# Kernel tuning notes

Measured on AMD Instinct MI355X. Metric: run time of the kernel, lower is better.

## Reference

```python
import jax, jax.numpy as jnp
import numpy as np

B, N, D_MODEL, H = 2, 512, 256, 8
DH, DS, DE = 8, 8, 8          # hyperbolic / spherical / euclidean component dims
HEAD = D_MODEL // H           # 32
HALF = HEAD // 2              # 16 rope frequencies
KAPPA_S = 1.0                 # spherical curvature
EPS = 1e-6


def setup_inputs() -> dict:
    key = jax.random.key(0)
    ks = jax.random.split(key, 10)
    h = jax.random.normal(ks[0], (B, N, D_MODEL), jnp.float32)
    # manifold coords: hyperbolic part inside Poincare ball, spherical part on unit sphere
    xh = 0.3 * jnp.tanh(jax.random.normal(ks[1], (B, N, DH), jnp.float32))
    xs_raw = jax.random.normal(ks[2], (B, N, DS), jnp.float32)
    xs = xs_raw / jnp.linalg.norm(xs_raw, axis=-1, keepdims=True)
    xe = jax.random.normal(ks[3], (B, N, DE), jnp.float32)
    x = jnp.concatenate([xh, xs, xe], axis=-1)
    def lin(k):
        return 0.05 * jax.random.normal(k, (D_MODEL, D_MODEL), jnp.float32)
    inp = dict(
        h=h, x=x,
        Wq=lin(ks[4]), bq=jnp.zeros((D_MODEL,), jnp.float32),
        Wk=lin(ks[5]), bk=jnp.zeros((D_MODEL,), jnp.float32),
        Wv=lin(ks[6]), bv=jnp.zeros((D_MODEL,), jnp.float32),
        Wo=lin(ks[7]), bo=jnp.zeros((D_MODEL,), jnp.float32),
        w_kernel=jnp.ones((H, 3), jnp.float32),   # torch init: ones(num_heads, num_comp)
        beta=jnp.ones((H,), jnp.float32),
        edge_bias=0.1 * jax.random.normal(ks[8], (B, 1, N, N), jnp.float32),
        node_mask=jnp.ones((B, N), bool),
    )
    return inp


def _pairwise_geometry(x):
    """Returns dh (B,N,N), sdot (B,N,N), de2 (B,N,N), dist (B,N,N)."""
    xh, xs, xe = x[..., :DH], x[..., DH:DH + DS], x[..., DH + DS:]
    # hyperbolic: Poincare-ball distance arccosh(1 + 2|a-b|^2 / ((1-|a|^2)(1-|b|^2)))
    dh2_num = jnp.sum((xh[:, :, None, :] - xh[:, None, :, :]) ** 2, -1)
    one_m = 1.0 - jnp.sum(xh * xh, -1)                               # (B,N)
    arg = 1.0 + 2.0 * dh2_num / (one_m[:, :, None] * one_m[:, None, :])
    dh = jnp.arccosh(jnp.maximum(arg, 1.0 + EPS))
    # spherical: arccos of dot (unit vectors); raw dot kept for the kernel term
    sdot = jnp.einsum('bnd,bmd->bnm', xs, xs)
    ds = jnp.arccos(jnp.clip(sdot, -1.0 + EPS, 1.0 - EPS)) / np.sqrt(KAPPA_S)
    # euclidean: squared distance (kernel uses -d^2; product dist uses d^2)
    de2 = jnp.sum((xe[:, :, None, :] - xe[:, None, :, :]) ** 2, -1)
    dist = jnp.sqrt(dh * dh + ds * ds + de2)
    return dh, sdot, de2, dist


def reference(h, x, Wq, bq, Wk, bk, Wv, bv, Wo, bo, w_kernel, beta, edge_bias, node_mask):
    scale = 1.0 / np.sqrt(HEAD)
    rope_freq = jnp.exp(-np.log(10000.0) * jnp.arange(HALF, dtype=jnp.float32) / HALF)

    def heads(t):  # (B,N,D) -> (B,H,N,head)
        return t.reshape(B, N, H, HEAD).transpose(0, 2, 1, 3)

    Q = heads(h @ Wq.T + bq)
    K = heads(h @ Wk.T + bk)
    V = heads(h @ Wv.T + bv)

    dh, sdot, de2, dist = _pairwise_geometry(x)

    # M-RoPE: rotate Q by pairwise angle theta_ij = omega * d_M(x_i, x_j)
    theta = dist[..., None] * rope_freq                  # (B,N,N,half)
    cos_t = jnp.cos(theta)[:, None]                      # (B,1,N,N,half)
    sin_t = jnp.sin(theta)[:, None]
    q1, q2 = Q[..., 0::2], Q[..., 1::2]                  # (B,H,N,half)
    k1, k2 = K[..., 0::2], K[..., 1::2]
    qk_same = q1[:, :, :, None, :] * k1[:, :, None, :, :] + q2[:, :, :, None, :] * k2[:, :, None, :, :]
    qk_cross = q1[:, :, :, None, :] * k2[:, :, None, :, :] - q2[:, :, :, None, :] * k1[:, :, None, :, :]
    attn = (cos_t * qk_same + sin_t * qk_cross).sum(-1) * scale   # (B,H,N,N)

    # geodesic kernel bias: per-component kernels [H:-d_H, S:k*a.b, E:-|a-b|^2]
    kernel_stack = jnp.stack([-dh, KAPPA_S * sdot, -de2], axis=-1)  # (B,N,N,3)
    geo = jnp.einsum('hc,bnmc->bhnm', w_kernel, kernel_stack)
    attn = attn + beta[None, :, None, None] * geo + edge_bias

    attn = jnp.where(node_mask[:, None, None, :], attn, -jnp.inf)
    p = jax.nn.softmax(attn, axis=-1)
    out = jnp.einsum('bhnm,bhmd->bhnd', p, V).transpose(0, 2, 1, 3).reshape(B, N, D_MODEL)
    return out @ Wo.T + bo
```

## Files before the change

### kernel.cpp

```cpp
#include <hip/hip_runtime.h>

#define N_TOK 512
#define NH 8

typedef __attribute__((ext_vector_type(8))) short short8;
typedef __attribute__((ext_vector_type(4))) short short4v;
typedef __attribute__((ext_vector_type(4))) float f32x4;

__device__ __forceinline__ unsigned short f2bf(float f) {
    union { float f; unsigned u; } v; v.f = f;
    return (unsigned short)((v.u + 0x7FFF + ((v.u >> 16) & 1)) >> 16);
}

__global__ __launch_bounds__(256) void gemm_qkv_mfma(
    const float* __restrict__ A,
    const float* __restrict__ Wq, const float* __restrict__ Wk, const float* __restrict__ Wv,
    const float* __restrict__ bq, const float* __restrict__ bk, const float* __restrict__ bv,
    float* __restrict__ Qb, float* __restrict__ KR, float* __restrict__ Vb)
{
    const int bx = blockIdx.x;
    const int t = threadIdx.x;
    const int z = bx >> 8, rem = bx & 255;
    const int m0 = (rem >> 3) * 32, n0 = (rem & 7) * 32;
    const float* W    = (z == 0) ? Wq : (z == 1) ? Wk : Wv;
    const float* bias = (z == 0) ? bq : (z == 1) ? bk : bv;

    __shared__ short As[32][264];
    __shared__ short Ws[32][264];

    #pragma unroll
    for (int r = 0; r < 8; ++r) {
        int idx = t + 256 * r;
        int row = idx >> 6, c4 = (idx & 63) * 4;
        float4 a = *(const float4*)&A[(m0 + row) * 256 + c4];
        short4v pa = {(short)f2bf(a.x), (short)f2bf(a.y), (short)f2bf(a.z), (short)f2bf(a.w)};
        *(short4v*)&As[row][c4] = pa;
        float4 w = *(const float4*)&W[(n0 + row) * 256 + c4];
        short4v pw = {(short)f2bf(w.x), (short)f2bf(w.y), (short)f2bf(w.z), (short)f2bf(w.w)};
        *(short4v*)&Ws[row][c4] = pw;
    }
    __syncthreads();

    const int w = t >> 6, lane = t & 63;
    const int wm = (w >> 1) * 16, wn = (w & 1) * 16;
    const int frow = lane & 15, kq = lane >> 4;

    f32x4 acc = {0.f, 0.f, 0.f, 0.f};
    #pragma unroll
    for (int k0 = 0; k0 < 8; ++k0) {
        short8 af = *(const short8*)&As[wm + frow][k0 * 32 + kq * 8];
        short8 wf = *(const short8*)&Ws[wn + frow][k0 * 32 + kq * 8];
        if (z == 1) acc = __builtin_amdgcn_mfma_f32_16x16x32_bf16(wf, af, acc, 0, 0, 0);
        else        acc = __builtin_amdgcn_mfma_f32_16x16x32_bf16(af, wf, acc, 0, 0, 0);
    }
    const int col = lane & 15, rq = (lane >> 4) * 4;
    if (z == 1) {
        int tok = m0 + wm + col;
        int bb = tok >> 9, j = tok & 511;
        #pragma unroll
        for (int r = 0; r < 4; ++r) {
            int d = n0 + wn + rq + r;
            int h = d >> 5, dd = d & 31, f = dd >> 1, r2 = dd & 1;
            KR[((size_t)bb * 128 + h * 16 + f) * 1024 + j * 2 + r2] = acc[r] + bias[d];
        }
    } else {
        float* C = (z == 0) ? Qb : Vb;
        float bsv = bias[n0 + wn + col];
        #pragma unroll
        for (int r = 0; r < 4; ++r)
            C[(m0 + wm + rq + r) * 256 + n0 + wn + col] = acc[r] + bsv;
    }
}

__global__ __launch_bounds__(256) void geo_kernel(
    const float* __restrict__ x, float* __restrict__ geo)
{
    const int j0 = blockIdx.x * 256;
    const int i  = blockIdx.y;
    const int b  = blockIdx.z;
    const int t  = threadIdx.x;

    __shared__ float xls[256 * 25];
    const float4* xsrc = (const float4*)(x + ((size_t)b * N_TOK + j0) * 24);
    #pragma unroll
    for (int r = 0; r < 6; ++r) {
        int idx = t + 256 * r;
        float4 v = xsrc[idx];
        int row = idx / 6, c = (idx % 6) * 4;
        float* dst = &xls[row * 25 + c];
        dst[0] = v.x; dst[1] = v.y; dst[2] = v.z; dst[3] = v.w;
    }
    const float* xi = x + ((size_t)b * N_TOK + i) * 24;
    float onemi = 1.0f;
    #pragma unroll
    for (int k = 0; k < 8; ++k) onemi -= xi[k] * xi[k];
    __syncthreads();

    const float* xr = &xls[t * 25];
    float dh2 = 0.f, oj = 0.f, sd = 0.f, de2 = 0.f;
    #pragma unroll
    for (int k = 0; k < 8; ++k) { float xj = xr[k]; float d = xi[k] - xj; dh2 += d * d; oj += xj * xj; }
    #pragma unroll
    for (int k = 0; k < 8; ++k) sd += xi[8 + k] * xr[8 + k];
    #pragma unroll
    for (int k = 0; k < 8; ++k) { float d = xi[16 + k] - xr[16 + k]; de2 += d * d; }
    float arg = 1.0f + 2.0f * dh2 / (onemi * (1.0f - oj));
    arg = fmaxf(arg, 1.0f + 1e-6f);
    float dh = __logf(arg + sqrtf(arg * arg - 1.0f));
    float sdc = fminf(fmaxf(sd, -1.0f + 1e-6f), 1.0f - 1e-6f);
    float dsp = acosf(sdc);
    float dist = sqrtf(dh * dh + dsp * dsp + de2);

    size_t idx = ((size_t)b * N_TOK + i) * N_TOK + j0 + t;
    geo[idx]               = dh;
    geo[idx +     524288]  = sd;
    geo[idx + 2 * 524288]  = de2;
    geo[idx + 3 * 524288]  = dist;
}

__global__ __launch_bounds__(256, 4) void attn_kernel(
    const float* __restrict__ Q, const float* __restrict__ KR, const float* __restrict__ V,
    const float* __restrict__ geo, const float* __restrict__ eb,
    const float* __restrict__ wker, const float* __restrict__ beta,
    float* __restrict__ Ao)
{
    const float FRQ[16] = {
        1.0f, 0.5623413251903491f, 0.31622776601683794f, 0.17782794100389228f,
        0.1f, 0.05623413251903491f, 0.031622776601683794f, 0.017782794100389228f,
        0.01f, 0.005623413251903491f, 0.0031622776601683794f, 0.0017782794100389228f,
        0.001f, 0.0005623413251903491f, 0.00031622776601683795f, 0.00017782794100389228f};

    const int t = threadIdx.x;
    const int lane = t & 63;
    const int wv = t >> 6;
    const int wid = blockIdx.x * 4 + wv;
    const int b  = __builtin_amdgcn_readfirstlane(wid >> 11);
    const int h  = __builtin_amdgcn_readfirstlane((wid >> 8) & 7);
    const int ip = __builtin_amdgcn_readfirstlane(wid & 255);
    const int i0 = ip * 2;

    __shared__ float es[4][2][128];

    const float* q0p = Q + ((size_t)b * N_TOK + i0) * 256 + h * 32;
    const float* q1p = q0p + 256;
    const float wk0 = wker[h * 3 + 0], wk1 = wker[h * 3 + 1], wk2 = wker[h * 3 + 2];
    const float bet = beta[h];
    const float scale = 0.17677669529663687f;

    const size_t gbase = ((size_t)b * N_TOK + i0) * N_TOK;
    const float* kbase = KR + ((size_t)b * 128 + h * 16) * 1024;

    float dsum[2] = {0.f, 0.f};
    float acc[2][4] = {{0.f,0.f,0.f,0.f},{0.f,0.f,0.f,0.f}};
    const int jsub = lane >> 3, dq = lane & 7;

    for (int tile = 0; tile < 4; ++tile) {
        const int j0 = tile * 128;
        float2 gdh[2], gsd[2], gde[2], gds[2];
        #pragma unroll
        for (int ii = 0; ii < 2; ++ii) {
            size_t gi = gbase + (size_t)ii * N_TOK + j0 + 2 * lane;
            gdh[ii] = *(const float2*)&geo[gi];
            gsd[ii] = *(const float2*)&geo[gi + 524288];
            gde[ii] = *(const float2*)&geo[gi + 2 * 524288];
            gds[ii] = *(const float2*)&geo[gi + 3 * 524288];
        }
        float dot[2][2] = {{0.f, 0.f}, {0.f, 0.f}};
        #pragma unroll
        for (int fg = 0; fg < 2; ++fg) {
            float4 kv[8];
            #pragma unroll
            for (int fl = 0; fl < 8; ++fl)
                kv[fl] = *(const float4*)&kbase[(size_t)(fg * 8 + fl) * 1024 + (j0 + 2 * lane) * 2];
            #pragma unroll
            for (int fl = 0; fl < 8; ++fl) {
                const int f = fg * 8 + fl;
                const float frq = FRQ[f];
                float4 kk = kv[fl];
                #pragma unroll
                for (int ii = 0; ii < 2; ++ii) {
                    const float* qp = ii ? q1p : q0p;
                    float q1 = qp[f * 2], q2 = qp[f * 2 + 1];
                    float c0, s0, c1, s1;
                    __sincosf(gds[ii].x * frq, &s0, &c0);
                    __sincosf(gds[ii].y * frq, &s1, &c1);
                    float t1 = q1 * kk.x + q2 * kk.y;
                    float t2 = q1 * kk.y - q2 * kk.x;
                    dot[ii][0] += c0 * t1 + s0 * t2;
                    t1 = q1 * kk.z + q2 * kk.w;
                    t2 = q1 * kk.w - q2 * kk.z;
                    dot[ii][1] += c1 * t1 + s1 * t2;
                }
            }
        }
        #pragma unroll
        for (int ii = 0; ii < 2; ++ii) {
            float2 e2 = *(const float2*)&eb[((size_t)b * N_TOK + i0 + ii) * N_TOK + j0 + 2 * lane];
            float bias0 = bet * (wk1 * gsd[ii].x - wk0 * gdh[ii].x - wk2 * gde[ii].x) + e2.x;
            float bias1 = bet * (wk1 * gsd[ii].y - wk0 * gdh[ii].y - wk2 * gde[ii].y) + e2.y;
            float e0 = __expf(dot[ii][0] * scale + bias0);
            float e1 = __expf(dot[ii][1] * scale + bias1);
            dsum[ii] += e0 + e1;
            *(float2*)&es[wv][ii][2 * lane] = make_float2(e0, e1);
        }
        {
            const float* vp = V + ((size_t)b * N_TOK + j0 + jsub) * 256 + h * 32 + dq * 4;
            #pragma unroll
            for (int it = 0; it < 16; ++it) {
                float4 v4 = *(const float4*)&vp[(size_t)it * 8 * 256];
                int j = it * 8 + jsub;
                float e0 = es[wv][0][j], e1 = es[wv][1][j];
                acc[0][0] += e0 * v4.x; acc[0][1] += e0 * v4.y;
                acc[0][2] += e0 * v4.z; acc[0][3] += e0 * v4.w;
                acc[1][0] += e1 * v4.x; acc[1][1] += e1 * v4.y;
                acc[1][2] += e1 * v4.z; acc[1][3] += e1 * v4.w;
            }
        }
    }

    #pragma unroll
    for (int ii = 0; ii < 2; ++ii) {
        float v = dsum[ii];
        v += __shfl_xor(v, 1);  v += __shfl_xor(v, 2);  v += __shfl_xor(v, 4);
        v += __shfl_xor(v, 8);  v += __shfl_xor(v, 16); v += __shfl_xor(v, 32);
        dsum[ii] = 1.0f / v;
    }
    #pragma unroll
    for (int ii = 0; ii < 2; ++ii)
        #pragma unroll
        for (int dd = 0; dd < 4; ++dd) {
            float a = acc[ii][dd];
            a += __shfl_xor(a, 8); a += __shfl_xor(a, 16); a += __shfl_xor(a, 32);
            acc[ii][dd] = a;
        }
    if (jsub == 0) {
        #pragma unroll
        for (int ii = 0; ii < 2; ++ii) {
            float4 o;
            o.x = acc[ii][0] * dsum[ii]; o.y = acc[ii][1] * dsum[ii];
            o.z = acc[ii][2] * dsum[ii]; o.w = acc[ii][3] * dsum[ii];
            *(float4*)&Ao[((size_t)b * N_TOK + i0 + ii) * 256 + h * 32 + dq * 4] = o;
        }
    }
}

__global__ __launch_bounds__(256) void gemm_out_mfma(
    const float* __restrict__ Ao, const float* __restrict__ Wo,
    const float* __restrict__ bo, float* __restrict__ out)
{
    const int t = threadIdx.x;
    const int m0 = (blockIdx.x >> 3) * 32, n0 = (blockIdx.x & 7) * 32;

    __shared__ short As[32][264];
    __shared__ short Ws[32][264];

    #pragma unroll
    for (int r = 0; r < 8; ++r) {
        int idx = t + 256 * r;
        int row = idx >> 6, c4 = (idx & 63) * 4;
        float4 a = *(const float4*)&Ao[(m0 + row) * 256 + c4];
        short4v pa = {(short)f2bf(a.x), (short)f2bf(a.y), (short)f2bf(a.z), (short)f2bf(a.w)};
        *(short4v*)&As[row][c4] = pa;
        float4 w = *(const float4*)&Wo[(n0 + row) * 256 + c4];
        short4v pw = {(short)f2bf(w.x), (short)f2bf(w.y), (short)f2bf(w.z), (short)f2bf(w.w)};
        *(short4v*)&Ws[row][c4] = pw;
    }
    __syncthreads();

    const int w = t >> 6, lane = t & 63;
    const int wm = (w >> 1) * 16, wn = (w & 1) * 16;
    const int frow = lane & 15, kq = lane >> 4;

    f32x4 acc = {0.f, 0.f, 0.f, 0.f};
    #pragma unroll
    for (int k0 = 0; k0 < 8; ++k0) {
        short8 af = *(const short8*)&As[wm + frow][k0 * 32 + kq * 8];
        short8 wf = *(const short8*)&Ws[wn + frow][k0 * 32 + kq * 8];
        acc = __builtin_amdgcn_mfma_f32_16x16x32_bf16(af, wf, acc, 0, 0, 0);
    }
    const int col = lane & 15, rq = (lane >> 4) * 4;
    float bsv = bo[n0 + wn + col];
    #pragma unroll
    for (int r = 0; r < 4; ++r)
        out[(m0 + wm + rq + r) * 256 + n0 + wn + col] = acc[r] + bsv;
}

extern "C" void kernel_launch(void* const* d_in, const int* in_sizes, int n_in,
                              void* d_out, int out_size, void* d_ws, size_t ws_size,
                              hipStream_t stream) {
    const float* hin  = (const float*)d_in[0];
    const float* x    = (const float*)d_in[1];
    const float* Wq   = (const float*)d_in[2];
    const float* bq   = (const float*)d_in[3];
    const float* Wk   = (const float*)d_in[4];
    const float* bk   = (const float*)d_in[5];
    const float* Wv   = (const float*)d_in[6];
    const float* bv   = (const float*)d_in[7];
    const float* Wo   = (const float*)d_in[8];
    const float* bo   = (const float*)d_in[9];
    const float* wker = (const float*)d_in[10];
    const float* beta = (const float*)d_in[11];
    const float* eb   = (const float*)d_in[12];
    float* out = (float*)d_out;
    float* w   = (float*)d_ws;

    float* Qb  = w;
    float* KR  = w + 262144;
    float* Vb  = w + 524288;
    float* Ao  = w + 786432;
    float* geo = w + 1048576;

    hipLaunchKernelGGL(gemm_qkv_mfma, dim3(768), dim3(256), 0, stream,
                       hin, Wq, Wk, Wv, bq, bk, bv, Qb, KR, Vb);
    hipLaunchKernelGGL(geo_kernel, dim3(2, 512, 2), dim3(256), 0, stream,
                       x, geo);
    hipLaunchKernelGGL(attn_kernel, dim3(1024), dim3(256), 0, stream,
                       Qb, KR, Vb, geo, eb, wker, beta, Ao);
    hipLaunchKernelGGL(gemm_out_mfma, dim3(256), dim3(256), 0, stream,
                       Ao, Wo, bo, out);
}
```

Measured before the change: 138.0 us.

## Split attention key range across two waves and use native sin/cos

Each attention wave now covers half of the key range, which doubles the grid to 2048 blocks and raises the occupancy hint to 8. Partial numerators and denominators go to workspace and are combined and normalised in the output GEMM's load stage. The geometry kernel pre-divides the distance by 2π, so attention can apply a fractional range reduction and call the hardware sin/cos instructions instead of __sincosf. This adds extra workspace traffic for the partial sums, and the higher occupancy target may force register spills.

```diff
diff --git a/kernel.cpp b/kernel.cpp
--- a/kernel.cpp
+++ b/kernel.cpp
@@ -115,14 +115,14 @@
     geo[idx]               = dh;
     geo[idx +     524288]  = sd;
     geo[idx + 2 * 524288]  = de2;
-    geo[idx + 3 * 524288]  = dist;
-}
-
-__global__ __launch_bounds__(256, 4) void attn_kernel(
+    geo[idx + 3 * 524288]  = dist * 0.15915494309189535f;
+}
+
+__global__ __launch_bounds__(256, 8) void attn_kernel(
     const float* __restrict__ Q, const float* __restrict__ KR, const float* __restrict__ V,
     const float* __restrict__ geo, const float* __restrict__ eb,
     const float* __restrict__ wker, const float* __restrict__ beta,
-    float* __restrict__ Ao)
+    float* __restrict__ num, float* __restrict__ den)
 {
     const float FRQ[16] = {
         1.0f, 0.5623413251903491f, 0.31622776601683794f, 0.17782794100389228f,
@@ -134,9 +134,10 @@
     const int lane = t & 63;
     const int wv = t >> 6;
     const int wid = blockIdx.x * 4 + wv;
-    const int b  = __builtin_amdgcn_readfirstlane(wid >> 11);
-    const int h  = __builtin_amdgcn_readfirstlane((wid >> 8) & 7);
-    const int ip = __builtin_amdgcn_readfirstlane(wid & 255);
+    const int b  = __builtin_amdgcn_readfirstlane(wid >> 12);
+    const int h  = __builtin_amdgcn_readfirstlane((wid >> 9) & 7);
+    const int ip = __builtin_amdgcn_readfirstlane((wid >> 1) & 255);
+    const int jh = __builtin_amdgcn_readfirstlane(wid & 1);
     const int i0 = ip * 2;
 
     __shared__ float es[4][2][128];
@@ -154,8 +155,8 @@
     float acc[2][4] = {{0.f,0.f,0.f,0.f},{0.f,0.f,0.f,0.f}};
     const int jsub = lane >> 3, dq = lane & 7;
 
-    for (int tile = 0; tile < 4; ++tile) {
-        const int j0 = tile * 128;
+    for (int tile = 0; tile < 2; ++tile) {
+        const int j0 = jh * 256 + tile * 128;
         float2 gdh[2], gsd[2], gde[2], gds[2];
         #pragma unroll
         for (int ii = 0; ii < 2; ++ii) {
@@ -181,9 +182,10 @@
                 for (int ii = 0; ii < 2; ++ii) {
                     const float* qp = ii ? q1p : q0p;
                     float q1 = qp[f * 2], q2 = qp[f * 2 + 1];
-                    float c0, s0, c1, s1;
-                    __sincosf(gds[ii].x * frq, &s0, &c0);
-                    __sincosf(gds[ii].y * frq, &s1, &c1);
+                    float r0 = gds[ii].x * frq; r0 -= floorf(r0);
+                    float r1 = gds[ii].y * frq; r1 -= floorf(r1);
+                    float s0 = __builtin_amdgcn_sinf(r0), c0 = __builtin_amdgcn_cosf(r0);
+                    float s1 = __builtin_amdgcn_sinf(r1), c1 = __builtin_amdgcn_cosf(r1);
                     float t1 = q1 * kk.x + q2 * kk.y;
                     float t2 = q1 * kk.y - q2 * kk.x;
                     dot[ii][0] += c0 * t1 + s0 * t2;
@@ -223,7 +225,7 @@
         float v = dsum[ii];
         v += __shfl_xor(v, 1);  v += __shfl_xor(v, 2);  v += __shfl_xor(v, 4);
         v += __shfl_xor(v, 8);  v += __shfl_xor(v, 16); v += __shfl_xor(v, 32);
-        dsum[ii] = 1.0f / v;
+        dsum[ii] = v;
     }
     #pragma unroll
     for (int ii = 0; ii < 2; ++ii)
@@ -233,20 +235,24 @@
             a += __shfl_xor(a, 8); a += __shfl_xor(a, 16); a += __shfl_xor(a, 32);
             acc[ii][dd] = a;
         }
+    float* nump = num + (size_t)jh * 262144;
+    float* denp = den + (size_t)jh * 8192;
+    if (lane == 0) {
+        denp[((size_t)b * N_TOK + i0) * 8 + h]     = dsum[0];
+        denp[((size_t)b * N_TOK + i0 + 1) * 8 + h] = dsum[1];
+    }
     if (jsub == 0) {
         #pragma unroll
         for (int ii = 0; ii < 2; ++ii) {
-            float4 o;
-            o.x = acc[ii][0] * dsum[ii]; o.y = acc[ii][1] * dsum[ii];
-            o.z = acc[ii][2] * dsum[ii]; o.w = acc[ii][3] * dsum[ii];
-            *(float4*)&Ao[((size_t)b * N_TOK + i0 + ii) * 256 + h * 32 + dq * 4] = o;
+            float4 o; o.x = acc[ii][0]; o.y = acc[ii][1]; o.z = acc[ii][2]; o.w = acc[ii][3];
+            *(float4*)&num[(size_t)jh * 262144 + ((size_t)b * N_TOK + i0 + ii) * 256 + h * 32 + dq * 4] = o;
         }
     }
 }
 
 __global__ __launch_bounds__(256) void gemm_out_mfma(
-    const float* __restrict__ Ao, const float* __restrict__ Wo,
-    const float* __restrict__ bo, float* __restrict__ out)
+    const float* __restrict__ num, const float* __restrict__ den,
+    const float* __restrict__ Wo, const float* __restrict__ bo, float* __restrict__ out)
 {
     const int t = threadIdx.x;
     const int m0 = (blockIdx.x >> 3) * 32, n0 = (blockIdx.x & 7) * 32;
@@ -258,8 +264,14 @@
     for (int r = 0; r < 8; ++r) {
         int idx = t + 256 * r;
         int row = idx >> 6, c4 = (idx & 63) * 4;
-        float4 a = *(const float4*)&Ao[(m0 + row) * 256 + c4];
-        short4v pa = {(short)f2bf(a.x), (short)f2bf(a.y), (short)f2bf(a.z), (short)f2bf(a.w)};
+        int m = m0 + row;
+        float4 a0 = *(const float4*)&num[(size_t)m * 256 + c4];
+        float4 a1 = *(const float4*)&num[262144 + (size_t)m * 256 + c4];
+        int hh = c4 >> 5;
+        float dsum = den[m * 8 + hh] + den[8192 + m * 8 + hh];
+        float inv = 1.0f / dsum;
+        short4v pa = {(short)f2bf((a0.x + a1.x) * inv), (short)f2bf((a0.y + a1.y) * inv),
+                      (short)f2bf((a0.z + a1.z) * inv), (short)f2bf((a0.w + a1.w) * inv)};
         *(short4v*)&As[row][c4] = pa;
         float4 w = *(const float4*)&Wo[(n0 + row) * 256 + c4];
         short4v pw = {(short)f2bf(w.x), (short)f2bf(w.y), (short)f2bf(w.z), (short)f2bf(w.w)};
@@ -307,15 +319,16 @@
     float* Qb  = w;
     float* KR  = w + 262144;
     float* Vb  = w + 524288;
-    float* Ao  = w + 786432;
-    float* geo = w + 1048576;
+    float* num = w + 786432;
+    float* den = w + 1310720;
+    float* geo = w + 1327104;
 
     hipLaunchKernelGGL(gemm_qkv_mfma, dim3(768), dim3(256), 0, stream,
                        hin, Wq, Wk, Wv, bq, bk, bv, Qb, KR, Vb);
     hipLaunchKernelGGL(geo_kernel, dim3(2, 512, 2), dim3(256), 0, stream,
                        x, geo);
-    hipLaunchKernelGGL(attn_kernel, dim3(1024), dim3(256), 0, stream,
-                       Qb, KR, Vb, geo, eb, wker, beta, Ao);
+    hipLaunchKernelGGL(attn_kernel, dim3(2048), dim3(256), 0, stream,
+                       Qb, KR, Vb, geo, eb, wker, beta, num, den);
     hipLaunchKernelGGL(gemm_out_mfma, dim3(256), dim3(256), 0, stream,
-                       Ao, Wo, bo, out);
-}
+                       num, den, Wo, bo, out);
+}
```

Measured after the change: 200.4 us. +45.3%, slower.
